# Performance work log

Measured on AMD Instinct MI355X. Metric: run time of the kernel, lower is better.

## Reference

```python
import jax, jax.numpy as jnp
import numpy as np

B, S, HID = 2, 2048, 2048
NH, NKV, HD = 16, 4, 128
GROUPS = NH // NKV
ROPE_BASE = 10000.0


def setup_inputs() -> dict:
    key = jax.random.key(0)
    ks = jax.random.split(key, 12)

    def w(k, i, o):
        return (jax.random.normal(k, (i, o), jnp.float32) * (i ** -0.5)).astype(jnp.float32)

    return {
        'x_real': jax.random.normal(ks[0], (B, S, HID), jnp.float32),
        'x_imag': jax.random.normal(ks[1], (B, S, HID), jnp.float32),
        'Wq_r': w(ks[2], HID, HID), 'Wq_i': w(ks[3], HID, HID),
        'bq_r': jnp.zeros((HID,), jnp.float32), 'bq_i': jnp.zeros((HID,), jnp.float32),
        'Wk_r': w(ks[4], HID, NKV * HD), 'Wk_i': w(ks[5], HID, NKV * HD),
        'bk_r': jnp.zeros((NKV * HD,), jnp.float32), 'bk_i': jnp.zeros((NKV * HD,), jnp.float32),
        'Wv_r': w(ks[6], HID, NKV * HD), 'Wv_i': w(ks[7], HID, NKV * HD),
        'bv_r': jnp.zeros((NKV * HD,), jnp.float32), 'bv_i': jnp.zeros((NKV * HD,), jnp.float32),
        'Wo_r': w(ks[8], HID, HID), 'Wo_i': w(ks[9], HID, HID),
        'bo_r': jnp.zeros((HID,), jnp.float32), 'bo_i': jnp.zeros((HID,), jnp.float32),
    }


def _clinear(xr, xi, Wr, Wi, br, bi):
    # complex linear: (xr + i*xi) @ (Wr + i*Wi) + (br + i*bi)
    out_r = xr @ Wr - xi @ Wi + br
    out_i = xr @ Wi + xi @ Wr + bi
    return out_r, out_i


def _split_heads(xr, xi, n_heads):
    b, s, _ = xr.shape
    xr = xr.reshape(b, s, n_heads, -1).transpose(0, 2, 1, 3)  # [B,H,S,D]
    xi = xi.reshape(b, s, n_heads, -1).transpose(0, 2, 1, 3)
    return xr, xi


def _rope(xr, xi):
    # complex rotary embedding: multiply (xr + i*xi) by exp(i * pos * inv_freq)
    s, d = xr.shape[-2], xr.shape[-1]
    inv_freq = 1.0 / (ROPE_BASE ** (jnp.arange(0, d, 2, dtype=jnp.float32) / d))
    freqs = jnp.arange(s, dtype=jnp.float32)[:, None] * inv_freq[None, :]  # [S, D/2]
    emb = jnp.concatenate([freqs, freqs], axis=-1)  # [S, D]
    cos, sin = jnp.cos(emb), jnp.sin(emb)
    return xr * cos - xi * sin, xr * sin + xi * cos


def _repeat_kv(xr, xi):
    if GROUPS == 1:
        return xr, xi
    b, hkv, s, d = xr.shape
    xr = jnp.broadcast_to(xr[:, :, None], (b, hkv, GROUPS, s, d)).reshape(b, NH, s, d)
    xi = jnp.broadcast_to(xi[:, :, None], (b, hkv, GROUPS, s, d)).reshape(b, NH, s, d)
    return xr, xi


def reference(x_real, x_imag, Wq_r, Wq_i, bq_r, bq_i, Wk_r, Wk_i, bk_r, bk_i,
              Wv_r, Wv_i, bv_r, bv_i, Wo_r, Wo_i, bo_r, bo_i):
    q_r, q_i = _clinear(x_real, x_imag, Wq_r, Wq_i, bq_r, bq_i)
    k_r, k_i = _clinear(x_real, x_imag, Wk_r, Wk_i, bk_r, bk_i)
    v_r, v_i = _clinear(x_real, x_imag, Wv_r, Wv_i, bv_r, bv_i)

    q_r, q_i = _split_heads(q_r, q_i, NH)
    k_r, k_i = _split_heads(k_r, k_i, NKV)
    v_r, v_i = _split_heads(v_r, v_i, NKV)

    q_r, q_i = _rope(q_r, q_i)
    k_r, k_i = _rope(k_r, k_i)

    k_r, k_i = _repeat_kv(k_r, k_i)
    v_r, v_i = _repeat_kv(v_r, v_i)

    scale = 1.0 / jnp.sqrt(jnp.float32(HD))
    # real part of complex inner product q . conj(k)
    scores = (jnp.einsum('bhqd,bhkd->bhqk', q_r, k_r)
              + jnp.einsum('bhqd,bhkd->bhqk', q_i, k_i)) * scale
    s = scores.shape[-1]
    causal = jnp.tril(jnp.ones((s, s), bool))
    scores = jnp.where(causal, scores, jnp.float32(-1e9))
    attn = jax.nn.softmax(scores, axis=-1)  # [B,H,S,S]

    out_r = jnp.einsum('bhqk,bhkd->bhqd', attn, v_r)
    out_i = jnp.einsum('bhqk,bhkd->bhqd', attn, v_i)

    # merge heads
    b = out_r.shape[0]
    out_r = out_r.transpose(0, 2, 1, 3).reshape(b, s, NH * HD)
    out_i = out_i.transpose(0, 2, 1, 3).reshape(b, s, NH * HD)

    out_r, out_i = _clinear(out_r, out_i, Wo_r, Wo_i, bo_r, bo_i)
    return out_r, out_i, attn
```

## Files before the change

### kernel.cpp

```cpp
#include <hip/hip_runtime.h>
#include <hip/hip_bf16.h>

#define S_LEN 2048
#define HIDDEN 2048
#define NHEAD 16
#define NKVH 4
#define HEADD 128
#define BATCH 2

typedef __attribute__((ext_vector_type(4))) float f32x4;
typedef __attribute__((ext_vector_type(8))) short bf16x8;
typedef __attribute__((ext_vector_type(4))) unsigned short u16x4;

__device__ __forceinline__ unsigned short f2bf(float f) {
  union { __hip_bfloat16 h; unsigned short u; } cv;
  cv.h = __float2bfloat16(f);
  return cv.u;
}

__device__ __forceinline__ float bf2f(unsigned short u) {
  union { float f; unsigned int i; } cv;
  cv.i = (unsigned int)u << 16;
  return cv.f;
}

__device__ __forceinline__ void gl_lds16(const void* g, void* l) {
  __builtin_amdgcn_global_load_lds(
      (const __attribute__((address_space(1))) unsigned int*)g,
      (__attribute__((address_space(3))) unsigned int*)l,
      16, 0, 0);
}

__device__ __forceinline__ f32x4 mfma16(bf16x8 a, bf16x8 b, f32x4 c) {
  return __builtin_amdgcn_mfma_f32_16x16x32_bf16(a, b, c, 0, 0, 0);
}

__global__ void k_rope_table(float* tab) {
  int idx = blockIdx.x * blockDim.x + threadIdx.x;
  if (idx >= S_LEN * 64) return;
  int s = idx >> 6, j = idx & 63;
  float invf = expf(-(float)j * (logf(10000.0f) / 64.0f));
  float ang = (float)s * invf;
  float sn, cs;
  sincosf(ang, &sn, &cs);
  tab[idx * 2 + 0] = cs;
  tab[idx * 2 + 1] = sn;
}

__global__ void k_pack_x(const float* __restrict__ xr, const float* __restrict__ xi,
                         unsigned short* __restrict__ Xp) {
  int idx = blockIdx.x * blockDim.x + threadIdx.x;
  if (idx >= 4096 * 4096 / 4) return;
  int m = idx >> 10;
  int c4 = idx & 1023;
  const float* src = (c4 < 512) ? (xr + (size_t)m * 2048 + c4 * 4)
                                : (xi + (size_t)m * 2048 + (c4 - 512) * 4);
  f32x4 v = *(const f32x4*)src;
  ((u16x4*)Xp)[idx] = (u16x4){f2bf(v.x), f2bf(v.y), f2bf(v.z), f2bf(v.w)};
}

__global__ void k_pack_w(const float* __restrict__ wq_r, const float* __restrict__ wq_i,
                         const float* __restrict__ wk_r, const float* __restrict__ wk_i,
                         const float* __restrict__ wv_r, const float* __restrict__ wv_i,
                         const float* __restrict__ wo_r, const float* __restrict__ wo_i,
                         unsigned short* __restrict__ Wt) {
  __shared__ float tile[32][33];
  int k0 = blockIdx.x * 32;
  int n0 = blockIdx.y * 32;
  int tx = threadIdx.x, ty0 = threadIdx.y;
#pragma unroll
  for (int i = 0; i < 4; ++i) {
    int ty = ty0 + i * 8;
    int k = k0 + ty;
    int n = n0 + tx;
    const float* Wr; const float* Wi; int w, t, part, j;
    if (n < 4096)      { Wr = wq_r; Wi = wq_i; w = 2048; t = n;        }
    else if (n < 5120) { Wr = wk_r; Wi = wk_i; w = 512;  t = n - 4096; }
    else if (n < 6144) { Wr = wv_r; Wi = wv_i; w = 512;  t = n - 5120; }
    else               { Wr = wo_r; Wi = wo_i; w = 2048; t = n - 6144; }
    part = (t >= w); j = part ? (t - w) : t;
    float v;
    if (part == 0) v = (k < 2048) ? Wr[(size_t)k * w + j] : -Wi[(size_t)(k - 2048) * w + j];
    else           v = (k < 2048) ? Wi[(size_t)k * w + j] :  Wr[(size_t)(k - 2048) * w + j];
    tile[ty][tx] = v;
  }
  __syncthreads();
#pragma unroll
  for (int i = 0; i < 4; ++i) {
    int ty = ty0 + i * 8;
    Wt[(size_t)(n0 + ty) * 4096 + k0 + tx] = f2bf(tile[tx][ty]);
  }
}

template <int MODE>
__global__ __launch_bounds__(512, 2) void k_gemm256(
    const unsigned short* __restrict__ A, const unsigned short* __restrict__ Bt,
    float* __restrict__ C, int ldc, int NTN,
    float* __restrict__ outR, float* __restrict__ outI,
    const float* __restrict__ bR, const float* __restrict__ bI) {
  constexpr int KD = 4096;
  constexpr int Kb = KD * 2;
  constexpr int NT = KD / 64;
  constexpr int NITER = NT / 2;
  __shared__ __align__(16) char smem[131072];
  int tid = threadIdx.x, lane = tid & 63, wid = tid >> 6;
  int wm = wid >> 2, wn = wid & 3;
  int nwg = gridDim.x;
  int bid = blockIdx.x;
  int swz = (bid & 7) * (nwg >> 3) + (bid >> 3);
  int mt = swz / NTN, nt = swz - mt * NTN;
  int m0 = mt * 256, n0 = nt * 256;

  const char* Ab = (const char*)A + (size_t)m0 * Kb;
  const char* Bb = (const char*)Bt + (size_t)n0 * Kb;
  char* L = smem;

  int i0 = tid, i1 = tid + 512;
  int pl0 = (i0 >> 3) * Kb + (((i0 & 7) ^ ((i0 >> 3) & 7)) << 4);
  int pl1 = (i1 >> 3) * Kb + (((i1 & 7) ^ ((i1 >> 3) & 7)) << 4);

  int jx0 = (((lane >> 4)) ^ (lane & 7)) << 4;
  int jx1 = (((lane >> 4) + 4) ^ (lane & 7)) << 4;
  int arow = (wm * 64 + (lane & 15)) * 128;
  int brow = (wn * 32 + (lane & 15)) * 128;

  auto STAGE_A = [&](int buf, int half, int kt) {
    const char* s = Ab + (size_t)half * 128 * Kb + kt * 128;
    char* d = L + buf * 32768 + half * 16384 + (wid << 10);
    gl_lds16(s + pl0, d);
    gl_lds16(s + pl1, d + 8192);
  };
  auto STAGE_B = [&](int buf, int half, int kt) {
    const char* s = Bb + (size_t)half * 128 * Kb + kt * 128;
    char* d = L + 65536 + buf * 32768 + half * 16384 + (wid << 10);
    gl_lds16(s + pl0, d);
    gl_lds16(s + pl1, d + 8192);
  };
  auto LD_A = [&](bf16x8* dst, int buf, int half) {
    const char* base = L + buf * 32768 + half * 16384 + arow;
#pragma unroll
    for (int mf = 0; mf < 4; ++mf) {
      dst[mf * 2 + 0] = *(const bf16x8*)(base + mf * 2048 + jx0);
      dst[mf * 2 + 1] = *(const bf16x8*)(base + mf * 2048 + jx1);
    }
  };
  auto LD_B = [&](bf16x8* dst, int buf, int half) {
    const char* base = L + 65536 + buf * 32768 + half * 16384 + brow;
#pragma unroll
    for (int nf = 0; nf < 2; ++nf) {
      dst[nf * 2 + 0] = *(const bf16x8*)(base + nf * 2048 + jx0);
      dst[nf * 2 + 1] = *(const bf16x8*)(base + nf * 2048 + jx1);
    }
  };

  f32x4 acc[8][4];
  const f32x4 fz = {0.f, 0.f, 0.f, 0.f};
#pragma unroll
  for (int i = 0; i < 8; ++i)
#pragma unroll
    for (int j = 0; j < 4; ++j) acc[i][j] = fz;

  bf16x8 aX[8], aY[8], bX[4], bY[4];

#define BARR() __builtin_amdgcn_s_barrier()
#define WAITV(drain) do { if (drain) asm volatile("s_waitcnt vmcnt(0)" ::: "memory"); \
                          else       asm volatile("s_waitcnt vmcnt(6)" ::: "memory"); } while (0)
#define MMQ(aS, bS, qm, qn) do { \
    __builtin_amdgcn_s_setprio(1); \
    _Pragma("unroll") \
    for (int mf = 0; mf < 4; ++mf) \
      _Pragma("unroll") \
      for (int nf = 0; nf < 2; ++nf) { \
        acc[(qm)*4+mf][(qn)*2+nf] = mfma16(aS[mf*2+0], bS[nf*2+0], acc[(qm)*4+mf][(qn)*2+nf]); \
        acc[(qm)*4+mf][(qn)*2+nf] = mfma16(aS[mf*2+1], bS[nf*2+1], acc[(qm)*4+mf][(qn)*2+nf]); \
      } \
    __builtin_amdgcn_s_setprio(0); \
  } while (0)

  STAGE_A(0, 0, 0);
  STAGE_B(0, 0, 0);
  STAGE_B(0, 1, 0);
  STAGE_A(0, 1, 0);
  STAGE_A(1, 0, 1);
  STAGE_B(1, 0, 1);
  STAGE_B(1, 1, 1);
  asm volatile("s_waitcnt vmcnt(6)" ::: "memory");
  BARR();

  for (int it = 0; it < NITER; ++it) {
    int t1 = 2 * it + 1, t2 = 2 * it + 2, t3 = 2 * it + 3;
    bool nl = (it < NITER - 1);
    LD_A(aX, 0, 0); LD_B(bX, 0, 0);
    STAGE_A(1, 1, t1);
    BARR(); MMQ(aX, bX, 0, 0); BARR();
    LD_B(bY, 0, 1);
    if (nl) STAGE_A(0, 0, t2);
    BARR(); MMQ(aX, bY, 0, 1); BARR();
    LD_A(aY, 0, 1);
    if (nl) STAGE_B(0, 0, t2);
    BARR(); MMQ(aY, bY, 1, 1); BARR();
    if (nl) STAGE_B(0, 1, t2);
    WAITV(!nl); BARR(); MMQ(aY, bX, 1, 0); BARR();
    LD_A(aX, 1, 0); LD_B(bY, 1, 0);
    if (nl) STAGE_A(0, 1, t2);
    BARR(); MMQ(aX, bY, 0, 0); BARR();
    LD_B(bX, 1, 1);
    if (nl) STAGE_A(1, 0, t3);
    BARR(); MMQ(aX, bX, 0, 1); BARR();
    LD_A(aY, 1, 1);
    if (nl) STAGE_B(1, 0, t3);
    BARR(); MMQ(aY, bX, 1, 1); BARR();
    if (nl) STAGE_B(1, 1, t3);
    WAITV(!nl); BARR(); MMQ(aY, bY, 1, 0); BARR();
  }

  int r0 = (lane >> 4) << 2, col0 = lane & 15;
#pragma unroll
  for (int qm = 0; qm < 2; ++qm)
#pragma unroll
    for (int mf = 0; mf < 4; ++mf)
#pragma unroll
      for (int qn = 0; qn < 2; ++qn)
#pragma unroll
        for (int nf = 0; nf < 2; ++nf) {
          f32x4 v = acc[qm * 4 + mf][qn * 2 + nf];
          int rowb = m0 + qm * 128 + wm * 64 + mf * 16 + r0;
          int col = n0 + qn * 128 + wn * 32 + nf * 16 + col0;
#pragma unroll
          for (int r = 0; r < 4; ++r) {
            int row = rowb + r;
            if (MODE == 0) {
              C[(size_t)row * ldc + col] = v[r];
            } else {
              if (col < 2048) outR[(size_t)row * 2048 + col] = v[r] + bR[col];
              else            outI[(size_t)row * 2048 + (col - 2048)] = v[r] + bI[col - 2048];
            }
          }
        }
#undef BARR
#undef WAITV
#undef MMQ
}

__global__ __launch_bounds__(512, 1) void k_attn_fused(
    const unsigned short* __restrict__ Qcat, const unsigned short* __restrict__ Kcat,
    const unsigned short* __restrict__ Vt, float* __restrict__ attn,
    unsigned short* __restrict__ Cpack) {
  __shared__ __align__(16) char smem[148480];
  const float scale = 0.08838834764831845f;

  int tid = threadIdx.x, lane = tid & 63, wid = tid >> 6;
  int l15 = lane & 15, l4 = lane >> 4;
  int bid = blockIdx.x;
  int qt = 15 - (bid >> 5), bh = bid & 31;
  int b = bh >> 4, h = bh & 15;
  int nt = 2 * qt + 2;

  const char* Qb = (const char*)Qcat + (size_t)bh * S_LEN * 512 + (size_t)qt * 128 * 512;
  const char* Kb = (const char*)Kcat + (size_t)(b * NKVH + (h >> 2)) * S_LEN * 512;
  const char* Vb = (const char*)Vt + (size_t)(b * NKVH + (h >> 2)) * 256 * (size_t)S_LEN * 2;
  float* P = attn + (size_t)bh * S_LEN * S_LEN;

  int r5 = tid >> 5, c5 = tid & 31;
  int sw512 = ((c5 ^ (r5 & 7)) << 4);
  int r3 = tid >> 3, c3 = tid & 7;
  int sw128 = ((c3 ^ (r3 & 7)) << 4);
  char* ldst = smem + (wid << 10);

  auto stQ = [&]() {
#pragma unroll
    for (int c = 0; c < 8; ++c)
      gl_lds16(Qb + (size_t)(c * 16 + r5) * 512 + sw512, ldst + c * 8192);
  };
  auto stK = [&](int base, int kv0) {
#pragma unroll
    for (int c = 0; c < 4; ++c)
      gl_lds16(Kb + (size_t)(kv0 + c * 16 + r5) * 512 + sw512, ldst + base + c * 8192);
  };
  auto stV = [&](int kv0) {
#pragma unroll
    for (int c = 0; c < 4; ++c)
      gl_lds16(Vb + (size_t)(c * 64 + r3) * 4096 + kv0 * 2 + sw128,
               ldst + 98304 + c * 8192);
  };

  auto QKT = [&](f32x4 accs[2][2], int kbase) {
#pragma unroll
    for (int kf = 0; kf < 8; ++kf) {
      bf16x8 a[2], bb[2];
#pragma unroll
      for (int mf = 0; mf < 2; ++mf) {
        int row = (wid >> 1) * 32 + mf * 16 + l15;
        a[mf] = *(const bf16x8*)(smem + row * 512 + (((kf * 4 + l4) ^ (row & 7)) << 4));
      }
#pragma unroll
      for (int nf = 0; nf < 2; ++nf) {
        int row = (wid & 1) * 32 + nf * 16 + l15;
        bb[nf] = *(const bf16x8*)(smem + kbase + row * 512 + (((kf * 4 + l4) ^ (row & 7)) << 4));
      }
#pragma unroll
      for (int mf = 0; mf < 2; ++mf)
#pragma unroll
        for (int nf = 0; nf < 2; ++nf)
          accs[mf][nf] = mfma16(a[mf], bb[nf], accs[mf][nf]);
    }
  };

  float* sPart = (float*)(smem + 131072);
  float2* sML = (float2*)(smem + 147456);

#define BARL() do { asm volatile("s_waitcnt lgkmcnt(0)" ::: "memory"); \
                    __builtin_amdgcn_s_barrier(); } while (0)

  if (tid < 128) sML[tid] = make_float2(-1e30f, 0.f);
  stQ();
  stK(65536, 0);
  stK(98304, 64);
  asm volatile("s_waitcnt vmcnt(4)" ::: "memory");
  __builtin_amdgcn_s_barrier();

  for (int t = 0; t < nt; ++t) {
    int kbase = 65536 + (t & 1) * 32768;
    f32x4 accs[2][2];
#pragma unroll
    for (int i = 0; i < 2; ++i)
#pragma unroll
      for (int j = 0; j < 2; ++j) accs[i][j] = (f32x4){0.f, 0.f, 0.f, 0.f};
    QKT(accs, kbase);
    int kv0 = t * 64;
#pragma unroll
    for (int mf = 0; mf < 2; ++mf)
#pragma unroll
      for (int r = 0; r < 4; ++r) {
        int lrow = (wid >> 1) * 32 + mf * 16 + l4 * 4 + r;
        int grow = qt * 128 + lrow;
        int cA = kv0 + (wid & 1) * 32 + l15;
        float v0 = (cA <= grow) ? accs[mf][0][r] * scale : -1e30f;
        float v1 = (cA + 16 <= grow) ? accs[mf][1][r] * scale : -1e30f;
        float lm = fmaxf(v0, v1);
#pragma unroll
        for (int o = 1; o < 16; o <<= 1) lm = fmaxf(lm, __shfl_xor(lm, o));
        float ls = ((cA <= grow) ? __expf(v0 - lm) : 0.f) +
                   ((cA + 16 <= grow) ? __expf(v1 - lm) : 0.f);
#pragma unroll
        for (int o = 1; o < 16; o <<= 1) ls += __shfl_xor(ls, o);
        if (l15 == 0) {
          sPart[((wid & 1) * 128 + lrow) * 2 + 0] = lm;
          sPart[((wid & 1) * 128 + lrow) * 2 + 1] = ls;
        }
      }
    BARL();
    if (t + 2 < nt) stK(kbase, (t + 2) * 64);
    if (tid < 128) {
      float m0 = sPart[tid * 2], l0 = sPart[tid * 2 + 1];
      float m1 = sPart[(128 + tid) * 2], l1 = sPart[(128 + tid) * 2 + 1];
      float m01 = fmaxf(m0, m1);
      float l01 = l0 * __expf(m0 - m01) + l1 * __expf(m1 - m01);
      float2 old = sML[tid];
      float mn = fmaxf(old.x, m01);
      sML[tid] = make_float2(mn, old.y * __expf(old.x - mn) + l01 * __expf(m01 - mn));
    }
    BARL();
    if (t + 1 < nt) {
      if (t + 2 < nt) asm volatile("s_waitcnt vmcnt(4)" ::: "memory");
      else            asm volatile("s_waitcnt vmcnt(0)" ::: "memory");
      __builtin_amdgcn_s_barrier();
    }
  }
  if (tid < 128) {
    float2 ml = sML[tid];
    sML[tid] = make_float2(ml.x, 1.0f / ml.y);
  }
  BARL();

  stK(65536, 0);
  stV(0);
  asm volatile("s_waitcnt vmcnt(0)" ::: "memory");
  __builtin_amdgcn_s_barrier();

  int wmP = wid >> 2, wnP = wid & 3;
  f32x4 accp[4][4];
#pragma unroll
  for (int i = 0; i < 4; ++i)
#pragma unroll
    for (int j = 0; j < 4; ++j) accp[i][j] = (f32x4){0.f, 0.f, 0.f, 0.f};

  for (int t = 0; t < nt; ++t) {
    bool more = (t + 1 < nt);
    f32x4 accs[2][2];
#pragma unroll
    for (int i = 0; i < 2; ++i)
#pragma unroll
      for (int j = 0; j < 2; ++j) accs[i][j] = (f32x4){0.f, 0.f, 0.f, 0.f};
    QKT(accs, 65536);
    BARL();
    if (more) stK(65536, (t + 1) * 64);
    int kv0 = t * 64;
#pragma unroll
    for (int mf = 0; mf < 2; ++mf)
#pragma unroll
      for (int r = 0; r < 4; ++r) {
        int lrow = (wid >> 1) * 32 + mf * 16 + l4 * 4 + r;
        int grow = qt * 128 + lrow;
        float2 mi = sML[lrow];
#pragma unroll
        for (int nf = 0; nf < 2; ++nf) {
          int lcol = (wid & 1) * 32 + nf * 16 + l15;
          int gcol = kv0 + lcol;
          float s = accs[mf][nf][r] * scale;
          float p = (gcol <= grow) ? __expf(s - mi.x) * mi.y : 0.f;
          *(unsigned short*)(smem + 131072 + lrow * 128 +
                             (((lcol >> 3) ^ (lrow & 7)) << 4) + (lcol & 7) * 2) = f2bf(p);
        }
      }
    asm volatile("s_waitcnt lgkmcnt(0)" ::: "memory");
    if (more) asm volatile("s_waitcnt vmcnt(4)" ::: "memory");
    else      asm volatile("s_waitcnt vmcnt(0)" ::: "memory");
    __builtin_amdgcn_s_barrier();
#pragma unroll
    for (int p = 0; p < 4; ++p) {
      int row = p * 32 + wid * 4 + l4;
      int byte = 131072 + row * 128 + (((l15 >> 1) ^ (row & 7)) << 4) + (l15 & 1) * 8;
      u16x4 pv = *(const u16x4*)(smem + byte);
      f32x4 o = {bf2f(pv.x), bf2f(pv.y), bf2f(pv.z), bf2f(pv.w)};
      *(f32x4*)(P + (size_t)(qt * 128 + row) * S_LEN + kv0 + l15 * 4) = o;
    }
    __builtin_amdgcn_s_setprio(1);
#pragma unroll
    for (int ks = 0; ks < 2; ++ks) {
      bf16x8 a[4], bb[4];
#pragma unroll
      for (int mf = 0; mf < 4; ++mf) {
        int row = wmP * 64 + mf * 16 + l15;
        a[mf] = *(const bf16x8*)(smem + 131072 + row * 128 +
                                 (((ks * 4 + l4) ^ (row & 7)) << 4));
      }
#pragma unroll
      for (int nf = 0; nf < 4; ++nf) {
        int n = wnP * 64 + nf * 16 + l15;
        bb[nf] = *(const bf16x8*)(smem + 98304 + n * 128 +
                                  (((ks * 4 + l4) ^ (n & 7)) << 4));
      }
#pragma unroll
      for (int mf = 0; mf < 4; ++mf)
#pragma unroll
        for (int nf = 0; nf < 4; ++nf)
          accp[mf][nf] = mfma16(a[mf], bb[nf], accp[mf][nf]);
    }
    __builtin_amdgcn_s_setprio(0);
    BARL();
    if (more) {
      stV((t + 1) * 64);
      asm volatile("s_waitcnt vmcnt(8)" ::: "memory");
    }
    __builtin_amdgcn_s_barrier();
  }

  {
    int c0 = 128 * (qt + 1);
    const f32x4 z4 = {0.f, 0.f, 0.f, 0.f};
    for (int rr = 0; rr < 16; ++rr) {
      int grow = qt * 128 + wid * 16 + rr;
      for (int c = c0 + lane * 4; c < 2048; c += 256)
        *(f32x4*)(P + (size_t)grow * S_LEN + c) = z4;
    }
  }
  int r0w = l4 * 4;
#pragma unroll
  for (int mf = 0; mf < 4; ++mf)
#pragma unroll
    for (int nf = 0; nf < 4; ++nf) {
      int gmb = qt * 128 + wmP * 64 + mf * 16 + r0w;
      int nn = wnP * 64 + nf * 16 + l15;
      int gcol = (nn < 128) ? (h * 128 + nn) : (2048 + h * 128 + (nn - 128));
#pragma unroll
      for (int r = 0; r < 4; ++r)
        Cpack[(size_t)(b * S_LEN + gmb + r) * 4096 + gcol] = f2bf(accp[mf][nf][r]);
    }
#undef BARL
}

__global__ void k_rope_q(const float* __restrict__ QKVf, const float* __restrict__ tab,
                         const float* __restrict__ bqr, const float* __restrict__ bqi,
                         unsigned short* __restrict__ Qcat) {
  int idx = blockIdx.x * blockDim.x + threadIdx.x;
  if (idx >= BATCH * S_LEN * NHEAD * HEADD) return;
  int d = idx & 127;
  int h = (idx >> 7) & 15;
  int s = (idx >> 11) & 2047;
  int b = (idx >> 22) & 1;
  size_t m = (size_t)b * S_LEN + s;
  int colc = h * 128 + d;
  float qr = QKVf[m * 6144 + colc] + bqr[colc];
  float qi = QKVf[m * 6144 + 2048 + colc] + bqi[colc];
  int ti = (s * 64 + (d & 63)) * 2;
  float cs = tab[ti], sn = tab[ti + 1];
  float orr = qr * cs - qi * sn;
  float oii = qr * sn + qi * cs;
  size_t base = ((size_t)(b * NHEAD + h) * S_LEN + s) * 256;
  Qcat[base + d] = f2bf(orr);
  Qcat[base + 128 + d] = f2bf(oii);
}

__global__ void k_rope_k(const float* __restrict__ QKVf, const float* __restrict__ tab,
                         const float* __restrict__ bkr, const float* __restrict__ bki,
                         unsigned short* __restrict__ Kcat) {
  int idx = blockIdx.x * blockDim.x + threadIdx.x;
  if (idx >= BATCH * S_LEN * NKVH * HEADD) return;
  int d = idx & 127;
  int kv = (idx >> 7) & 3;
  int s = (idx >> 9) & 2047;
  int b = (idx >> 20) & 1;
  size_t m = (size_t)b * S_LEN + s;
  int jb = kv * 128 + d;
  float kr = QKVf[m * 6144 + 4096 + jb] + bkr[jb];
  float ki = QKVf[m * 6144 + 4608 + jb] + bki[jb];
  int ti = (s * 64 + (d & 63)) * 2;
  float cs = tab[ti], sn = tab[ti + 1];
  float orr = kr * cs - ki * sn;
  float oii = kr * sn + ki * cs;
  size_t base = ((size_t)(b * NKVH + kv) * S_LEN + s) * 256;
  Kcat[base + d] = f2bf(orr);
  Kcat[base + 128 + d] = f2bf(oii);
}

__global__ void k_vpack(const float* __restrict__ QKVf, const float* __restrict__ bvr,
                        const float* __restrict__ bvi, unsigned short* __restrict__ Vt) {
  __shared__ float tile[32][33];
  int s0 = blockIdx.x * 32, n0 = blockIdx.y * 32, bkv = blockIdx.z;
  int b = bkv >> 2, kv = bkv & 3;
  int tx = threadIdx.x, ty0 = threadIdx.y;
#pragma unroll
  for (int i = 0; i < 4; ++i) {
    int ty = ty0 + i * 8;
    int s = s0 + ty, n = n0 + tx;
    int d = n & 127, isI = n >> 7;
    int col = (isI ? 5632 : 5120) + kv * 128 + d;
    float bias = isI ? bvi[kv * 128 + d] : bvr[kv * 128 + d];
    tile[ty][tx] = QKVf[(size_t)(b * S_LEN + s) * 6144 + col] + bias;
  }
  __syncthreads();
#pragma unroll
  for (int i = 0; i < 4; ++i) {
    int ty = ty0 + i * 8;
    Vt[(size_t)(bkv * 256 + n0 + ty) * S_LEN + s0 + tx] = f2bf(tile[tx][ty]);
  }
}

extern "C" void kernel_launch(void* const* d_in, const int* in_sizes, int n_in,
                              void* d_out, int out_size, void* d_ws, size_t ws_size,
                              hipStream_t stream) {
  const float* xr = (const float*)d_in[0];
  const float* xi = (const float*)d_in[1];
  const float* wq_r = (const float*)d_in[2];
  const float* wq_i = (const float*)d_in[3];
  const float* bq_r = (const float*)d_in[4];
  const float* bq_i = (const float*)d_in[5];
  const float* wk_r = (const float*)d_in[6];
  const float* wk_i = (const float*)d_in[7];
  const float* bk_r = (const float*)d_in[8];
  const float* bk_i = (const float*)d_in[9];
  const float* wv_r = (const float*)d_in[10];
  const float* wv_i = (const float*)d_in[11];
  const float* bv_r = (const float*)d_in[12];
  const float* bv_i = (const float*)d_in[13];
  const float* wo_r = (const float*)d_in[14];
  const float* wo_i = (const float*)d_in[15];
  const float* bo_r = (const float*)d_in[16];
  const float* bo_i = (const float*)d_in[17];

  float* out = (float*)d_out;
  float* outR = out;
  float* outI = out + (size_t)BATCH * S_LEN * HIDDEN;
  float* attn = outI + (size_t)BATCH * S_LEN * HIDDEN;

  char* ws = (char*)d_ws;
  size_t off = 0;
  auto alloc = [&](size_t bytes) {
    char* p = ws + off;
    off += (bytes + 255) & ~(size_t)255;
    return p;
  };
  unsigned short* Xp = (unsigned short*)alloc((size_t)4096 * 4096 * 2);
  unsigned short* Wt = (unsigned short*)alloc((size_t)10240 * 4096 * 2);
  float* QKVf = (float*)alloc((size_t)4096 * 6144 * 4);
  float* tab = (float*)alloc((size_t)S_LEN * 64 * 2 * 4);
  unsigned short* Qcat = (unsigned short*)alloc((size_t)BATCH * NHEAD * S_LEN * 256 * 2);
  unsigned short* Kcat = (unsigned short*)alloc((size_t)BATCH * NKVH * S_LEN * 256 * 2);
  unsigned short* Vt = (unsigned short*)alloc((size_t)BATCH * NKVH * 256 * S_LEN * 2);
  unsigned short* Cpack = Xp;

  k_rope_table<<<512, 256, 0, stream>>>(tab);
  k_pack_x<<<16384, 256, 0, stream>>>(xr, xi, Xp);
  k_pack_w<<<dim3(128, 320), dim3(32, 8), 0, stream>>>(wq_r, wq_i, wk_r, wk_i, wv_r, wv_i,
                                                       wo_r, wo_i, Wt);
  k_gemm256<0><<<384, 512, 0, stream>>>(Xp, Wt, QKVf, 6144, 24,
                                        nullptr, nullptr, nullptr, nullptr);
  k_rope_q<<<32768, 256, 0, stream>>>(QKVf, tab, bq_r, bq_i, Qcat);
  k_rope_k<<<8192, 256, 0, stream>>>(QKVf, tab, bk_r, bk_i, Kcat);
  k_vpack<<<dim3(64, 8, 8), dim3(32, 8), 0, stream>>>(QKVf, bv_r, bv_i, Vt);
  k_attn_fused<<<512, 512, 0, stream>>>(Qcat, Kcat, Vt, attn, Cpack);
  k_gemm256<1><<<256, 512, 0, stream>>>(Cpack, Wt + (size_t)6144 * 4096, nullptr, 0, 16,
                                        outR, outI, bo_r, bo_i);
}
```

Measured before the change: 761.8 us.

## Fuse RoPE, bias and V transpose into QKV GEMM epilogue

Reorders the packed QKV weight columns so each 256-wide GEMM tile holds one head's real and imaginary halves. The QKV GEMM epilogue then adds the bias, applies RoPE for Q/K, or transposes V through shared memory, and writes the bf16 Qcat/Kcat/Vt buffers directly. This removes the fp32 QKV intermediate and three separate elementwise and transpose kernels. The cost is a heavier GEMM epilogue that uses swizzled LDS staging and an extra barrier.

```diff
diff --git a/kernel.cpp b/kernel.cpp
--- a/kernel.cpp
+++ b/kernel.cpp
@@ -73,12 +73,26 @@
     int ty = ty0 + i * 8;
     int k = k0 + ty;
     int n = n0 + tx;
-    const float* Wr; const float* Wi; int w, t, part, j;
-    if (n < 4096)      { Wr = wq_r; Wi = wq_i; w = 2048; t = n;        }
-    else if (n < 5120) { Wr = wk_r; Wi = wk_i; w = 512;  t = n - 4096; }
-    else if (n < 6144) { Wr = wv_r; Wi = wv_i; w = 512;  t = n - 5120; }
-    else               { Wr = wo_r; Wi = wo_i; w = 2048; t = n - 6144; }
-    part = (t >= w); j = part ? (t - w) : t;
+    const float* Wr; const float* Wi; int w, part, j;
+    if (n < 4096) {
+      Wr = wq_r; Wi = wq_i; w = 2048;
+      int h = n >> 8, p = (n >> 7) & 1, d = n & 127;
+      part = p; j = h * 128 + d;
+    } else if (n < 5120) {
+      Wr = wk_r; Wi = wk_i; w = 512;
+      int t = n - 4096;
+      int kv = t >> 8, p = (t >> 7) & 1, d = t & 127;
+      part = p; j = kv * 128 + d;
+    } else if (n < 6144) {
+      Wr = wv_r; Wi = wv_i; w = 512;
+      int t = n - 5120;
+      int kv = t >> 8, p = (t >> 7) & 1, d = t & 127;
+      part = p; j = kv * 128 + d;
+    } else {
+      Wr = wo_r; Wi = wo_i; w = 2048;
+      int t = n - 6144;
+      part = (t >= w); j = part ? (t - w) : t;
+    }
     float v;
     if (part == 0) v = (k < 2048) ? Wr[(size_t)k * w + j] : -Wi[(size_t)(k - 2048) * w + j];
     else           v = (k < 2048) ? Wi[(size_t)k * w + j] :  Wr[(size_t)(k - 2048) * w + j];
@@ -95,9 +109,15 @@
 template <int MODE>
 __global__ __launch_bounds__(512, 2) void k_gemm256(
     const unsigned short* __restrict__ A, const unsigned short* __restrict__ Bt,
-    float* __restrict__ C, int ldc, int NTN,
+    int NTN,
     float* __restrict__ outR, float* __restrict__ outI,
-    const float* __restrict__ bR, const float* __restrict__ bI) {
+    const float* __restrict__ bR, const float* __restrict__ bI,
+    const float* __restrict__ tab,
+    const float* __restrict__ bqr, const float* __restrict__ bqi,
+    const float* __restrict__ bkr, const float* __restrict__ bki,
+    const float* __restrict__ bvr, const float* __restrict__ bvi,
+    unsigned short* __restrict__ Qcat, unsigned short* __restrict__ Kcat,
+    unsigned short* __restrict__ VtP) {
   constexpr int KD = 4096;
   constexpr int Kb = KD * 2;
   constexpr int NT = KD / 64;
@@ -215,28 +235,107 @@
   }
 
   int r0 = (lane >> 4) << 2, col0 = lane & 15;
-#pragma unroll
-  for (int qm = 0; qm < 2; ++qm)
-#pragma unroll
-    for (int mf = 0; mf < 4; ++mf)
-#pragma unroll
-      for (int qn = 0; qn < 2; ++qn)
-#pragma unroll
-        for (int nf = 0; nf < 2; ++nf) {
-          f32x4 v = acc[qm * 4 + mf][qn * 2 + nf];
-          int rowb = m0 + qm * 128 + wm * 64 + mf * 16 + r0;
-          int col = n0 + qn * 128 + wn * 32 + nf * 16 + col0;
-#pragma unroll
-          for (int r = 0; r < 4; ++r) {
-            int row = rowb + r;
-            if (MODE == 0) {
-              C[(size_t)row * ldc + col] = v[r];
-            } else {
+
+  if (MODE == 1) {
+#pragma unroll
+    for (int qm = 0; qm < 2; ++qm)
+#pragma unroll
+      for (int mf = 0; mf < 4; ++mf)
+#pragma unroll
+        for (int qn = 0; qn < 2; ++qn)
+#pragma unroll
+          for (int nf = 0; nf < 2; ++nf) {
+            f32x4 v = acc[qm * 4 + mf][qn * 2 + nf];
+            int rowb = m0 + qm * 128 + wm * 64 + mf * 16 + r0;
+            int col = n0 + qn * 128 + wn * 32 + nf * 16 + col0;
+#pragma unroll
+            for (int r = 0; r < 4; ++r) {
+              int row = rowb + r;
               if (col < 2048) outR[(size_t)row * 2048 + col] = v[r] + bR[col];
               else            outI[(size_t)row * 2048 + (col - 2048)] = v[r] + bI[col - 2048];
             }
           }
+    return;
+  }
+
+  __syncthreads();
+  int bidx = m0 >> 11;
+  int s0 = m0 & 2047;
+
+  if (n0 < 5120) {
+    bool isQ = (n0 < 4096);
+    int hh = isQ ? (n0 >> 8) : ((n0 - 4096) >> 8);
+    const float* bRp = isQ ? bqr : bkr;
+    const float* bIp = isQ ? bqi : bki;
+    int jbase = hh * 128;
+#pragma unroll
+    for (int qm = 0; qm < 2; ++qm)
+#pragma unroll
+      for (int mf = 0; mf < 4; ++mf)
+#pragma unroll
+        for (int nf = 0; nf < 2; ++nf) {
+          int d = wn * 32 + nf * 16 + col0;
+          f32x4 vr = acc[qm * 4 + mf][0 * 2 + nf];
+          f32x4 vi = acc[qm * 4 + mf][1 * 2 + nf];
+          float br = bRp[jbase + d], bi = bIp[jbase + d];
+#pragma unroll
+          for (int r = 0; r < 4; ++r) {
+            int lrow = qm * 128 + wm * 64 + mf * 16 + r0 + r;
+            int s = s0 + lrow;
+            float2 cs = *(const float2*)(tab + ((size_t)s * 64 + (d & 63)) * 2);
+            float qr = vr[r] + br;
+            float qi = vi[r] + bi;
+            float orr = qr * cs.x - qi * cs.y;
+            float oii = qr * cs.y + qi * cs.x;
+            int swz4 = (lrow & 3) << 3;
+            int g0 = (d >> 3) ^ swz4;
+            int g1 = ((128 + d) >> 3) ^ swz4;
+            *(unsigned short*)(L + lrow * 512 + g0 * 16 + (d & 7) * 2) = f2bf(orr);
+            *(unsigned short*)(L + lrow * 512 + g1 * 16 + (d & 7) * 2) = f2bf(oii);
+          }
         }
+    __syncthreads();
+    char* dstb = isQ ? (char*)Qcat + ((size_t)(bidx * 16 + hh) * 2048 + s0) * 512
+                     : (char*)Kcat + ((size_t)(bidx * 4 + hh) * 2048 + s0) * 512;
+#pragma unroll
+    for (int i = 0; i < 16; ++i) {
+      int cid = tid + 512 * i;
+      int row = cid >> 5, c = cid & 31;
+      int g = c ^ ((row & 3) << 3);
+      *(f32x4*)(dstb + (size_t)row * 512 + c * 16) = *(const f32x4*)(L + row * 512 + g * 16);
+    }
+  } else {
+    int kv = (n0 - 5120) >> 8;
+#pragma unroll
+    for (int qm = 0; qm < 2; ++qm)
+#pragma unroll
+      for (int mf = 0; mf < 4; ++mf)
+#pragma unroll
+        for (int qn = 0; qn < 2; ++qn)
+#pragma unroll
+          for (int nf = 0; nf < 2; ++nf) {
+            int dloc = wn * 32 + nf * 16 + col0;
+            int nlocal = qn * 128 + dloc;
+            f32x4 v = acc[qm * 4 + mf][qn * 2 + nf];
+            float bias = (qn ? bvi : bvr)[kv * 128 + dloc];
+#pragma unroll
+            for (int r = 0; r < 4; ++r) {
+              int lrow = qm * 128 + wm * 64 + mf * 16 + r0 + r;
+              int g = (lrow >> 3) ^ (nlocal & 31);
+              *(unsigned short*)(L + nlocal * 512 + g * 16 + (lrow & 7) * 2) =
+                  f2bf(v[r] + bias);
+            }
+          }
+    __syncthreads();
+    char* dstb = (char*)VtP + (size_t)(bidx * 4 + kv) * 256 * 4096 + (size_t)s0 * 2;
+#pragma unroll
+    for (int i = 0; i < 16; ++i) {
+      int cid = tid + 512 * i;
+      int n = cid >> 5, c = cid & 31;
+      int g = c ^ (n & 31);
+      *(f32x4*)(dstb + (size_t)n * 4096 + c * 16) = *(const f32x4*)(L + n * 512 + g * 16);
+    }
+  }
 #undef BARR
 #undef WAITV
 #undef MMQ
@@ -478,73 +577,6 @@
         Cpack[(size_t)(b * S_LEN + gmb + r) * 4096 + gcol] = f2bf(accp[mf][nf][r]);
     }
 #undef BARL
-}
-
-__global__ void k_rope_q(const float* __restrict__ QKVf, const float* __restrict__ tab,
-                         const float* __restrict__ bqr, const float* __restrict__ bqi,
-                         unsigned short* __restrict__ Qcat) {
-  int idx = blockIdx.x * blockDim.x + threadIdx.x;
-  if (idx >= BATCH * S_LEN * NHEAD * HEADD) return;
-  int d = idx & 127;
-  int h = (idx >> 7) & 15;
-  int s = (idx >> 11) & 2047;
-  int b = (idx >> 22) & 1;
-  size_t m = (size_t)b * S_LEN + s;
-  int colc = h * 128 + d;
-  float qr = QKVf[m * 6144 + colc] + bqr[colc];
-  float qi = QKVf[m * 6144 + 2048 + colc] + bqi[colc];
-  int ti = (s * 64 + (d & 63)) * 2;
-  float cs = tab[ti], sn = tab[ti + 1];
-  float orr = qr * cs - qi * sn;
-  float oii = qr * sn + qi * cs;
-  size_t base = ((size_t)(b * NHEAD + h) * S_LEN + s) * 256;
-  Qcat[base + d] = f2bf(orr);
-  Qcat[base + 128 + d] = f2bf(oii);
-}
-
-__global__ void k_rope_k(const float* __restrict__ QKVf, const float* __restrict__ tab,
-                         const float* __restrict__ bkr, const float* __restrict__ bki,
-                         unsigned short* __restrict__ Kcat) {
-  int idx = blockIdx.x * blockDim.x + threadIdx.x;
-  if (idx >= BATCH * S_LEN * NKVH * HEADD) return;
-  int d = idx & 127;
-  int kv = (idx >> 7) & 3;
-  int s = (idx >> 9) & 2047;
-  int b = (idx >> 20) & 1;
-  size_t m = (size_t)b * S_LEN + s;
-  int jb = kv * 128 + d;
-  float kr = QKVf[m * 6144 + 4096 + jb] + bkr[jb];
-  float ki = QKVf[m * 6144 + 4608 + jb] + bki[jb];
-  int ti = (s * 64 + (d & 63)) * 2;
-  float cs = tab[ti], sn = tab[ti + 1];
-  float orr = kr * cs - ki * sn;
-  float oii = kr * sn + ki * cs;
-  size_t base = ((size_t)(b * NKVH + kv) * S_LEN + s) * 256;
-  Kcat[base + d] = f2bf(orr);
-  Kcat[base + 128 + d] = f2bf(oii);
-}
-
-__global__ void k_vpack(const float* __restrict__ QKVf, const float* __restrict__ bvr,
-                        const float* __restrict__ bvi, unsigned short* __restrict__ Vt) {
-  __shared__ float tile[32][33];
-  int s0 = blockIdx.x * 32, n0 = blockIdx.y * 32, bkv = blockIdx.z;
-  int b = bkv >> 2, kv = bkv & 3;
-  int tx = threadIdx.x, ty0 = threadIdx.y;
-#pragma unroll
-  for (int i = 0; i < 4; ++i) {
-    int ty = ty0 + i * 8;
-    int s = s0 + ty, n = n0 + tx;
-    int d = n & 127, isI = n >> 7;
-    int col = (isI ? 5632 : 5120) + kv * 128 + d;
-    float bias = isI ? bvi[kv * 128 + d] : bvr[kv * 128 + d];
-    tile[ty][tx] = QKVf[(size_t)(b * S_LEN + s) * 6144 + col] + bias;
-  }
-  __syncthreads();
-#pragma unroll
-  for (int i = 0; i < 4; ++i) {
-    int ty = ty0 + i * 8;
-    Vt[(size_t)(bkv * 256 + n0 + ty) * S_LEN + s0 + tx] = f2bf(tile[tx][ty]);
-  }
 }
 
 extern "C" void kernel_launch(void* const* d_in, const int* in_sizes, int n_in,
@@ -583,7 +615,6 @@
   };
   unsigned short* Xp = (unsigned short*)alloc((size_t)4096 * 4096 * 2);
   unsigned short* Wt = (unsigned short*)alloc((size_t)10240 * 4096 * 2);
-  float* QKVf = (float*)alloc((size_t)4096 * 6144 * 4);
   float* tab = (float*)alloc((size_t)S_LEN * 64 * 2 * 4);
   unsigned short* Qcat = (unsigned short*)alloc((size_t)BATCH * NHEAD * S_LEN * 256 * 2);
   unsigned short* Kcat = (unsigned short*)alloc((size_t)BATCH * NKVH * S_LEN * 256 * 2);
@@ -594,12 +625,13 @@
   k_pack_x<<<16384, 256, 0, stream>>>(xr, xi, Xp);
   k_pack_w<<<dim3(128, 320), dim3(32, 8), 0, stream>>>(wq_r, wq_i, wk_r, wk_i, wv_r, wv_i,
                                                        wo_r, wo_i, Wt);
-  k_gemm256<0><<<384, 512, 0, stream>>>(Xp, Wt, QKVf, 6144, 24,
-                                        nullptr, nullptr, nullptr, nullptr);
-  k_rope_q<<<32768, 256, 0, stream>>>(QKVf, tab, bq_r, bq_i, Qcat);
-  k_rope_k<<<8192, 256, 0, stream>>>(QKVf, tab, bk_r, bk_i, Kcat);
-  k_vpack<<<dim3(64, 8, 8), dim3(32, 8), 0, stream>>>(QKVf, bv_r, bv_i, Vt);
+  k_gemm256<2><<<384, 512, 0, stream>>>(Xp, Wt, 24,
+                                        nullptr, nullptr, nullptr, nullptr,
+                                        tab, bq_r, bq_i, bk_r, bk_i, bv_r, bv_i,
+                                        Qcat, Kcat, Vt);
   k_attn_fused<<<512, 512, 0, stream>>>(Qcat, Kcat, Vt, attn, Cpack);
-  k_gemm256<1><<<256, 512, 0, stream>>>(Cpack, Wt + (size_t)6144 * 4096, nullptr, 0, 16,
-                                        outR, outI, bo_r, bo_i);
-}
+  k_gemm256<1><<<256, 512, 0, stream>>>(Cpack, Wt + (size_t)6144 * 4096, 16,
+                                        outR, outI, bo_r, bo_i,
+                                        nullptr, nullptr, nullptr, nullptr, nullptr,
+                                        nullptr, nullptr, nullptr, nullptr, nullptr);
+}
```

After: 729.5 us. 4.2% less time.
